# Performance work log

Hardware: AMD Instinct MI355X
Metric: run time of the kernel (lower is better)

## Reference

```python
import jax, jax.numpy as jnp
import numpy as np

B, S, HID = 2, 2048, 2048
H, KV, D = 16, 4, 128
EPS = 1e-6


def rms_norm(x, w, eps=EPS):
    # Qwen3.5 convention: (1 + weight) * RMSNorm(x), weight init 0
    v = jnp.mean(x * x, axis=-1, keepdims=True)
    return (1.0 + w) * (x * jax.lax.rsqrt(v + eps))


def rotate_half(x):
    x1, x2 = jnp.split(x, 2, axis=-1)
    return jnp.concatenate([-x2, x1], axis=-1)


def apply_rope(x, cos, sin):
    # x: [B,S,h,D]; cos/sin: [S,D]
    c = cos[None, :, None, :]
    s = sin[None, :, None, :]
    return x * c + rotate_half(x) * s


def setup_inputs():
    key = jax.random.key(0)
    ks = jax.random.split(key, 8)
    sc = 0.02
    hidden_states = jax.random.normal(ks[0], (B, S, HID), jnp.float32)
    past_key_value = jnp.zeros((B, 2, KV, S, D), jnp.float32)
    pos = jnp.arange(S, dtype=jnp.float32)
    inv_freq = 1.0 / (10000.0 ** (jnp.arange(0, D, 2, dtype=jnp.float32) / D))
    ang = pos[:, None] * inv_freq[None, :]                    # [S, D/2]
    cos = jnp.concatenate([jnp.cos(ang), jnp.cos(ang)], -1)   # [S, D]
    sin = jnp.concatenate([jnp.sin(ang), jnp.sin(ang)], -1)
    rope_rotary_cos_sin = jnp.stack([cos, sin], axis=1)       # [S, 2, D]
    context_lengths = jnp.full((B,), S, dtype=jnp.int32)
    kvcache_start_index = jnp.zeros((B,), dtype=jnp.int32)
    Wq = jax.random.normal(ks[1], (HID, H * D * 2), jnp.float32) * sc
    Wk = jax.random.normal(ks[2], (HID, KV * D), jnp.float32) * sc
    Wv = jax.random.normal(ks[3], (HID, KV * D), jnp.float32) * sc
    Wo = jax.random.normal(ks[4], (H * D, HID), jnp.float32) * sc
    q_norm_w = jax.random.normal(ks[5], (D,), jnp.float32) * sc
    k_norm_w = jax.random.normal(ks[6], (D,), jnp.float32) * sc
    return {"hidden_states": hidden_states, "past_key_value": past_key_value,
            "rope_rotary_cos_sin": rope_rotary_cos_sin,
            "context_lengths": context_lengths,
            "kvcache_start_index": kvcache_start_index,
            "Wq": Wq, "Wk": Wk, "Wv": Wv, "Wo": Wo,
            "q_norm_w": q_norm_w, "k_norm_w": k_norm_w}


def reference(hidden_states, past_key_value, rope_rotary_cos_sin,
              context_lengths, kvcache_start_index,
              Wq, Wk, Wv, Wo, q_norm_w, k_norm_w):
    # projections
    q_out = jnp.einsum('bsc,cd->bsd', hidden_states, Wq).reshape(B, S, H, 2 * D)
    query, gate = jnp.split(q_out, 2, axis=-1)                # each [B,S,H,D]
    k = jnp.einsum('bsc,cd->bsd', hidden_states, Wk).reshape(B, S, KV, D)
    v = jnp.einsum('bsc,cd->bsd', hidden_states, Wv).reshape(B, S, KV, D)
    # per-head QK RMSNorm
    query = rms_norm(query, q_norm_w)
    k = rms_norm(k, k_norm_w)
    # RoPE
    cos, sin = rope_rotary_cos_sin[:, 0, :], rope_rotary_cos_sin[:, 1, :]
    query = apply_rope(query, cos, sin)
    k = apply_rope(k, cos, sin)
    # write KV cache (prefill at start index 0)
    present = past_key_value.at[:, 0, :, :S, :].set(jnp.transpose(k, (0, 2, 1, 3)))
    present = present.at[:, 1, :, :S, :].set(jnp.transpose(v, (0, 2, 1, 3)))
    # GQA causal attention
    group = H // KV
    k_r = jnp.repeat(k, group, axis=2)                        # [B,S,H,D]
    v_r = jnp.repeat(v, group, axis=2)
    scores = jnp.einsum('bqhd,bkhd->bhqk', query, k_r) / jnp.sqrt(jnp.float32(D))
    causal = jnp.tril(jnp.ones((S, S), dtype=bool))
    scores = jnp.where(causal[None, None], scores, jnp.float32(-1e30))
    probs = jax.nn.softmax(scores, axis=-1)
    attn = jnp.einsum('bhqk,bkhd->bqhd', probs, v_r)          # [B,S,H,D]
    # sigmoid gating + output proj
    attn = attn * jax.nn.sigmoid(gate)
    out = jnp.einsum('bsd,dc->bsc', attn.reshape(B, S, H * D), Wo)
    return out, present
```

## Files before the change

### kernel.cpp

```cpp
#include <hip/hip_runtime.h>
#include <hip/hip_bf16.h>
#include <cstdint>
#include <cstddef>

#define BB   2
#define SS   2048
#define HIDD 2048
#define HH   16
#define KVH  4
#define DD   128
#define NQKV 5120
#define MM   4096

typedef unsigned short u16t;
typedef __attribute__((ext_vector_type(8))) short s16x8;
typedef __attribute__((ext_vector_type(4))) short s16x4;
typedef __attribute__((ext_vector_type(4))) float f32x4;

__device__ __forceinline__ u16t f2bf(float f) {
  unsigned u = __float_as_uint(f);
  u += 0x7fffu + ((u >> 16) & 1u);
  return (u16t)(u >> 16);
}
__device__ __forceinline__ float bf2f(u16t h) {
  return __uint_as_float(((unsigned)h) << 16);
}
__device__ __forceinline__ void gload_lds16(const void* g, void* l) {
  __builtin_amdgcn_global_load_lds(
      (const __attribute__((address_space(1))) unsigned int*)g,
      (__attribute__((address_space(3))) unsigned int*)l, 16, 0, 0);
}

__global__ __launch_bounds__(256) void cast_x(const float* __restrict__ in,
                                              u16t* __restrict__ out) {
  size_t i = ((size_t)blockIdx.x * 256 + threadIdx.x) * 4;
  f32x4 v = *(const f32x4*)(in + i);
  s16x4 o;
  o[0] = (short)f2bf(v[0]); o[1] = (short)f2bf(v[1]);
  o[2] = (short)f2bf(v[2]); o[3] = (short)f2bf(v[3]);
  *(s16x4*)(out + i) = o;
}

__global__ __launch_bounds__(256) void transpose_cast(const float* __restrict__ src,
                                                      u16t* __restrict__ dst, int N) {
  __shared__ float lds[64 * 65];
  int t = threadIdx.x;
  const int ktiles = HIDD / 64;
  int n0 = (blockIdx.x / ktiles) << 6;
  int k0 = (blockIdx.x % ktiles) << 6;
#pragma unroll
  for (int i = 0; i < 16; i++) {
    int idx = i * 256 + t;
    int r = idx >> 6, c = idx & 63;
    lds[c * 65 + r] = src[(size_t)(k0 + r) * N + n0 + c];
  }
  __syncthreads();
#pragma unroll
  for (int i = 0; i < 16; i++) {
    int idx = i * 256 + t;
    int rr = idx >> 6, kk = idx & 63;
    dst[(size_t)(n0 + rr) * HIDD + k0 + kk] = f2bf(lds[rr * 65 + kk]);
  }
}

__device__ __forceinline__ s16x8 ldsfrag(const char* half, int r, int g) {
  return *(const s16x8*)(half + r * 64 + ((g ^ ((r >> 1) & 3)) << 4));
}
__device__ __forceinline__ void stage_half(char* ldsbase, const u16t* gbase,
                                           int K, int kcol, int tid) {
#pragma unroll
  for (int i = 0; i < 2; i++) {
    int o16 = i * 512 + tid;
    int r = o16 >> 2;
    int cs = (o16 & 3) ^ ((r >> 1) & 3);
    gload_lds16(gbase + (size_t)r * K + kcol + cs * 8, ldsbase + o16 * 16);
  }
}

template <typename CT>
__global__ __launch_bounds__(512, 2) void gemm8(const u16t* __restrict__ A,
                                                const u16t* __restrict__ Bt,
                                                CT* __restrict__ C,
                                                int M, int N, int K) {
  extern __shared__ __align__(16) char lds[];
  char* As = lds;
  char* Bs = lds + 65536;
  int tid = threadIdx.x, lane = tid & 63, w = tid >> 6;
  int wm = w >> 2, wn = w & 3;
  int cpx = gridDim.x >> 3;
  int wgid = (blockIdx.x & 7) * cpx + (blockIdx.x >> 3);
  int bm = wgid & 15, bn = wgid >> 4;
  int m0 = bm << 8, n0 = bn << 8;
  const u16t* Ag = A + (size_t)m0 * K;
  const u16t* Bg = Bt + (size_t)n0 * K;
  const int NT = K >> 6;

  stage_half(As, Ag, K, 0, tid);
  stage_half(Bs, Bg, K, 0, tid);
  stage_half(As + 16384, Ag, K, 32, tid);
  stage_half(Bs + 16384, Bg, K, 32, tid);
  stage_half(As + 32768, Ag, K, 64, tid);
  stage_half(Bs + 32768, Bg, K, 64, tid);
  asm volatile("s_waitcnt vmcnt(8)" ::: "memory");
  __builtin_amdgcn_s_barrier();

  const f32x4 fz = {0.f, 0.f, 0.f, 0.f};
  f32x4 acc[8][4];
#pragma unroll
  for (int i = 0; i < 8; i++)
#pragma unroll
    for (int j = 0; j < 4; j++) acc[i][j] = fz;
  s16x8 afr[4], bfr[4];
  int g = lane >> 4;
  int rA = (lane & 15) + wm * 128;
  int rB = (lane & 15) + wn * 64;

  for (int kt = 0; kt < NT; kt++) {
    int cur = kt & 1;
    char* Acur = As + cur * 32768;
    char* Bcur = Bs + cur * 32768;
    char* Anxt = As + (cur ^ 1) * 32768;
    char* Bnxt = Bs + (cur ^ 1) * 32768;
#pragma unroll
    for (int ni = 0; ni < 4; ni++) bfr[ni] = ldsfrag(Bcur, rB + ni * 16, g);
#pragma unroll
    for (int mi = 0; mi < 4; mi++) afr[mi] = ldsfrag(Acur, rA + mi * 16, g);
    if (kt + 1 < NT) stage_half(Anxt + 16384, Ag, K, (kt + 1) * 64 + 32, tid);
    __builtin_amdgcn_s_barrier();
    asm volatile("s_waitcnt lgkmcnt(0)" ::: "memory");
    __builtin_amdgcn_s_setprio(1);
#pragma unroll
    for (int mi = 0; mi < 4; mi++)
#pragma unroll
      for (int ni = 0; ni < 4; ni++)
        acc[mi][ni] = __builtin_amdgcn_mfma_f32_16x16x32_bf16(afr[mi], bfr[ni], acc[mi][ni], 0, 0, 0);
    __builtin_amdgcn_s_setprio(0);
    __builtin_amdgcn_s_barrier();
#pragma unroll
    for (int mi = 0; mi < 4; mi++) afr[mi] = ldsfrag(Acur, rA + 64 + mi * 16, g);
    if (kt + 1 < NT) stage_half(Bnxt + 16384, Bg, K, (kt + 1) * 64 + 32, tid);
    __builtin_amdgcn_s_barrier();
    asm volatile("s_waitcnt lgkmcnt(0)" ::: "memory");
    __builtin_amdgcn_s_setprio(1);
#pragma unroll
    for (int mi = 0; mi < 4; mi++)
#pragma unroll
      for (int ni = 0; ni < 4; ni++)
        acc[4 + mi][ni] = __builtin_amdgcn_mfma_f32_16x16x32_bf16(afr[mi], bfr[ni], acc[4 + mi][ni], 0, 0, 0);
    __builtin_amdgcn_s_setprio(0);
    if (kt + 1 < NT) asm volatile("s_waitcnt vmcnt(8)" ::: "memory");
    else             asm volatile("s_waitcnt vmcnt(0)" ::: "memory");
    __builtin_amdgcn_s_barrier();
#pragma unroll
    for (int ni = 0; ni < 4; ni++) bfr[ni] = ldsfrag(Bcur + 16384, rB + ni * 16, g);
#pragma unroll
    for (int mi = 0; mi < 4; mi++) afr[mi] = ldsfrag(Acur + 16384, rA + mi * 16, g);
    if (kt + 2 < NT) stage_half(Acur, Ag, K, (kt + 2) * 64, tid);
    __builtin_amdgcn_s_barrier();
    asm volatile("s_waitcnt lgkmcnt(0)" ::: "memory");
    __builtin_amdgcn_s_setprio(1);
#pragma unroll
    for (int mi = 0; mi < 4; mi++)
#pragma unroll
      for (int ni = 0; ni < 4; ni++)
        acc[mi][ni] = __builtin_amdgcn_mfma_f32_16x16x32_bf16(afr[mi], bfr[ni], acc[mi][ni], 0, 0, 0);
    __builtin_amdgcn_s_setprio(0);
    __builtin_amdgcn_s_barrier();
#pragma unroll
    for (int mi = 0; mi < 4; mi++) afr[mi] = ldsfrag(Acur + 16384, rA + 64 + mi * 16, g);
    if (kt + 2 < NT) stage_half(Bcur, Bg, K, (kt + 2) * 64, tid);
    __builtin_amdgcn_s_barrier();
    asm volatile("s_waitcnt lgkmcnt(0)" ::: "memory");
    __builtin_amdgcn_s_setprio(1);
#pragma unroll
    for (int mi = 0; mi < 4; mi++)
#pragma unroll
      for (int ni = 0; ni < 4; ni++)
        acc[4 + mi][ni] = __builtin_amdgcn_mfma_f32_16x16x32_bf16(afr[mi], bfr[ni], acc[4 + mi][ni], 0, 0, 0);
    __builtin_amdgcn_s_setprio(0);
    if (kt < NT - 1) {
      if (kt + 2 < NT) asm volatile("s_waitcnt vmcnt(8)" ::: "memory");
      else             asm volatile("s_waitcnt vmcnt(4)" ::: "memory");
    }
    __builtin_amdgcn_s_barrier();
  }
#pragma unroll
  for (int mi = 0; mi < 8; mi++)
#pragma unroll
    for (int ni = 0; ni < 4; ni++) {
      int row0 = m0 + wm * 128 + mi * 16 + ((lane >> 4) << 2);
      int col = n0 + wn * 64 + ni * 16 + (lane & 15);
#pragma unroll
      for (int j = 0; j < 4; j++) {
        if constexpr (sizeof(CT) == 2)
          C[(size_t)(row0 + j) * N + col] = f2bf(acc[mi][ni][j]);
        else
          C[(size_t)(row0 + j) * N + col] = acc[mi][ni][j];
      }
    }
}

template <typename CT>
__global__ __launch_bounds__(256) void gemm_bt(const u16t* __restrict__ A,
                                               const u16t* __restrict__ Bt,
                                               CT* __restrict__ C,
                                               int M, int N, int K) {
  __shared__ __align__(16) char As[128 * 64];
  __shared__ __align__(16) char Bs[128 * 64];
  int tid = threadIdx.x;
  int lane = tid & 63;
  int w = tid >> 6;
  int cpx = gridDim.x >> 3;
  int wgid = ((int)blockIdx.x & 7) * cpx + ((int)blockIdx.x >> 3);
  int mtiles = M >> 7;
  int bm = wgid % mtiles;
  int bn = wgid / mtiles;
  int m0 = bm << 7, n0 = bn << 7;
  int wr = (w >> 1) * 64, wc = (w & 1) * 64;

  const f32x4 fz = {0.f, 0.f, 0.f, 0.f};
  f32x4 acc[4][4];
#pragma unroll
  for (int i = 0; i < 4; i++)
#pragma unroll
    for (int j = 0; j < 4; j++) acc[i][j] = fz;

  for (int k0 = 0; k0 < K; k0 += 32) {
    __syncthreads();
#pragma unroll
    for (int i = 0; i < 2; i++) {
      int idx = i * 256 + tid;
      int r = idx >> 2, c = idx & 3;
      int csrc = c ^ ((r >> 1) & 3);
      gload_lds16(A + (size_t)(m0 + r) * K + k0 + csrc * 8, As + idx * 16);
      gload_lds16(Bt + (size_t)(n0 + r) * K + k0 + csrc * 8, Bs + idx * 16);
    }
    __syncthreads();
    s16x8 af[4], bf[4];
    int g = lane >> 4;
#pragma unroll
    for (int mi = 0; mi < 4; mi++) {
      int r = wr + mi * 16 + (lane & 15);
      af[mi] = *(const s16x8*)(As + r * 64 + ((g ^ ((r >> 1) & 3)) << 4));
    }
#pragma unroll
    for (int ni = 0; ni < 4; ni++) {
      int r = wc + ni * 16 + (lane & 15);
      bf[ni] = *(const s16x8*)(Bs + r * 64 + ((g ^ ((r >> 1) & 3)) << 4));
    }
#pragma unroll
    for (int mi = 0; mi < 4; mi++)
#pragma unroll
      for (int ni = 0; ni < 4; ni++)
        acc[mi][ni] = __builtin_amdgcn_mfma_f32_16x16x32_bf16(af[mi], bf[ni], acc[mi][ni], 0, 0, 0);
  }
#pragma unroll
  for (int mi = 0; mi < 4; mi++)
#pragma unroll
    for (int ni = 0; ni < 4; ni++) {
      int row0 = m0 + wr + mi * 16 + ((lane >> 4) << 2);
      int col = n0 + wc + ni * 16 + (lane & 15);
#pragma unroll
      for (int j = 0; j < 4; j++) {
        if constexpr (sizeof(CT) == 2)
          C[(size_t)(row0 + j) * N + col] = f2bf(acc[mi][ni][j]);
        else
          C[(size_t)(row0 + j) * N + col] = acc[mi][ni][j];
      }
    }
}

__global__ __launch_bounds__(256) void qk_norm_rope(const u16t* __restrict__ Cqkv,
                                                    const float* __restrict__ rope,
                                                    const float* __restrict__ qw,
                                                    const float* __restrict__ kw,
                                                    u16t* __restrict__ Qb,
                                                    u16t* __restrict__ Kb,
                                                    u16t* __restrict__ Gs,
                                                    float* __restrict__ present) {
  int wid = blockIdx.x * 4 + (threadIdx.x >> 6);
  int lane = threadIdx.x & 63;
  const int NQ = BB * SS * HH;
  if (wid < NQ) {
    int b = wid >> 15;
    int rem = wid & 32767;
    int s = rem >> 4, h = rem & 15;
    const u16t* base = Cqkv + (size_t)(b * SS + s) * NQKV + h * 256;
    float xlo = bf2f(base[lane]), xhi = bf2f(base[64 + lane]);
    float ss = xlo * xlo + xhi * xhi;
    ss += __shfl_xor(ss, 1);  ss += __shfl_xor(ss, 2);  ss += __shfl_xor(ss, 4);
    ss += __shfl_xor(ss, 8);  ss += __shfl_xor(ss, 16); ss += __shfl_xor(ss, 32);
    float r = rsqrtf(ss * (1.f / 128.f) + 1e-6f);
    float qlo = xlo * r * (1.f + qw[lane]);
    float qhi = xhi * r * (1.f + qw[64 + lane]);
    const float* cs = rope + (size_t)s * 256;
    float clo = cs[lane], chi = cs[64 + lane];
    float slo = cs[128 + lane], shi = cs[192 + lane];
    const float SC = 0.08838834764831845f;
    float olo = (qlo * clo - qhi * slo) * SC;
    float ohi = (qhi * chi + qlo * shi) * SC;
    size_t qoff = (((size_t)b * HH + h) * SS + s) * DD;
    Qb[qoff + lane] = f2bf(olo);
    Qb[qoff + 64 + lane] = f2bf(ohi);
    float glo = bf2f(base[128 + lane]), ghi = bf2f(base[192 + lane]);
    size_t goff = ((size_t)(b * SS + s)) * (HH * DD) + h * DD;
    Gs[goff + lane] = f2bf(1.f / (1.f + __expf(-glo)));
    Gs[goff + 64 + lane] = f2bf(1.f / (1.f + __expf(-ghi)));
  } else {
    int wid2 = wid - NQ;
    int b = wid2 >> 13;
    int rem = wid2 & 8191;
    int s = rem >> 2, kv = rem & 3;
    const u16t* base = Cqkv + (size_t)(b * SS + s) * NQKV + 4096 + kv * 128;
    float xlo = bf2f(base[lane]), xhi = bf2f(base[64 + lane]);
    float ss = xlo * xlo + xhi * xhi;
    ss += __shfl_xor(ss, 1);  ss += __shfl_xor(ss, 2);  ss += __shfl_xor(ss, 4);
    ss += __shfl_xor(ss, 8);  ss += __shfl_xor(ss, 16); ss += __shfl_xor(ss, 32);
    float r = rsqrtf(ss * (1.f / 128.f) + 1e-6f);
    float klo = xlo * r * (1.f + kw[lane]);
    float khi = xhi * r * (1.f + kw[64 + lane]);
    const float* cs = rope + (size_t)s * 256;
    float clo = cs[lane], chi = cs[64 + lane];
    float slo = cs[128 + lane], shi = cs[192 + lane];
    float olo = klo * clo - khi * slo;
    float ohi = khi * chi + klo * shi;
    size_t koff = (((size_t)b * KVH + kv) * SS + s) * DD;
    Kb[koff + lane] = f2bf(olo);
    Kb[koff + 64 + lane] = f2bf(ohi);
    size_t poff = (((size_t)(b * 2 * KVH + kv)) * SS + s) * DD;
    present[poff + lane] = olo;
    present[poff + 64 + lane] = ohi;
  }
}

__global__ __launch_bounds__(256) void v_write(const u16t* __restrict__ Cqkv,
                                               float* __restrict__ present,
                                               u16t* __restrict__ Vtb) {
  __shared__ float lds[128 * 65];
  int t = threadIdx.x;
  int b = blockIdx.x >> 7;
  int kv = (blockIdx.x >> 5) & 3;
  int s0 = (blockIdx.x & 31) << 6;
#pragma unroll
  for (int i = 0; i < 32; i++) {
    int idx = i * 256 + t;
    int sp = idx >> 7, d = idx & 127;
    float v = bf2f(Cqkv[(size_t)(b * SS + s0 + sp) * NQKV + 4608 + kv * 128 + d]);
    present[(((size_t)(b * 2 * KVH + KVH + kv)) * SS + s0 + sp) * DD + d] = v;
    lds[d * 65 + sp] = v;
  }
  __syncthreads();
#pragma unroll
  for (int i = 0; i < 8; i++) {
    int d = i * 16 + (t >> 4);
    int sp = (t & 15) * 4;
    s16x4 pk;
    pk[0] = (short)f2bf(lds[d * 65 + sp + 0]);
    pk[1] = (short)f2bf(lds[d * 65 + sp + 1]);
    pk[2] = (short)f2bf(lds[d * 65 + sp + 2]);
    pk[3] = (short)f2bf(lds[d * 65 + sp + 3]);
    *(s16x4*)(Vtb + ((size_t)(b * KVH + kv) * DD + d) * SS + s0 + sp) = pk;
  }
}

__global__ __launch_bounds__(256) void attn_kernel(const u16t* __restrict__ Qb,
                                                   const u16t* __restrict__ Kb,
                                                   const u16t* __restrict__ Vtb,
                                                   const u16t* __restrict__ Gs,
                                                   u16t* __restrict__ AttG) {
  __shared__ __align__(16) char Ks[2][16384];
  __shared__ __align__(16) char Vs[2][16384];
  __shared__ __align__(16) char Ps[4 * 2048];

  int tid = threadIdx.x, lane = tid & 63, w = tid >> 6;
  int x = blockIdx.x & 7;
  int b = x >> 2, kv = x & 3;
  int rr = blockIdx.x >> 3;
  int h = kv * 4 + (rr & 3);
  int p = rr >> 2;

  const u16t* Kbase = Kb + (((size_t)(b * KVH + kv)) * SS) * DD;
  const u16t* Vbase = Vtb + (((size_t)(b * KVH + kv)) * DD) * SS;

  auto stageK = [&](int kt, int buf) {
#pragma unroll
    for (int i = 0; i < 4; i++) {
      int idx = i * 256 + tid;
      int r_ = idx >> 4, c_ = idx & 15;
      gload_lds16(Kbase + (size_t)(kt * 64 + r_) * DD + (c_ ^ (r_ & 7)) * 8, Ks[buf] + idx * 16);
    }
  };
  auto stageV = [&](int kt, int buf) {
#pragma unroll
    for (int i = 0; i < 4; i++) {
      int idx = i * 256 + tid;
      int r_ = idx >> 3, c_ = idx & 7;
      gload_lds16(Vbase + (size_t)r_ * SS + kt * 64 + (c_ ^ (r_ & 7)) * 8, Vs[buf] + idx * 16);
    }
  };

  const f32x4 fz = {0.f, 0.f, 0.f, 0.f};
  char* pbase = Ps + w * 2048;
  int cur = 0;

  stageK(0, 0);
  stageV(0, 0);

  for (int seg = 0; seg < 2; seg++) {
    int qt = (seg == 0) ? (31 - p) : p;
    const u16t* Qbase = Qb + (((size_t)(b * HH + h)) * SS + qt * 64) * DD;
    s16x8 qf[4];
    {
      const u16t* qrow = Qbase + (size_t)(w * 16 + (lane & 15)) * DD + (lane >> 4) * 8;
#pragma unroll
      for (int ks = 0; ks < 4; ks++) qf[ks] = *(const s16x8*)(qrow + ks * 32);
    }
    f32x4 acco[8];
#pragma unroll
    for (int f = 0; f < 8; f++) acco[f] = fz;
    float mrun[4], lrun[4];
#pragma unroll
    for (int j = 0; j < 4; j++) { mrun[j] = -INFINITY; lrun[j] = 0.f; }

    if (seg == 0) {
      asm volatile("s_waitcnt vmcnt(0)" ::: "memory");
      __builtin_amdgcn_s_barrier();
    }

    for (int kt = 0; kt <= qt; kt++) {
      bool havenext = (kt < qt) || (seg == 0);
      if (havenext) {
        int nk = (kt < qt) ? (kt + 1) : 0;
        stageK(nk, cur ^ 1);
        stageV(nk, cur ^ 1);
      }
      f32x4 accs[4];
#pragma unroll
      for (int ni = 0; ni < 4; ni++) accs[ni] = fz;
#pragma unroll
      for (int ni = 0; ni < 4; ni++) {
        int r = ni * 16 + (lane & 15);
#pragma unroll
        for (int ks = 0; ks < 4; ks++) {
          int g = ks * 4 + (lane >> 4);
          s16x8 bfk = *(const s16x8*)(Ks[cur] + r * 256 + ((g ^ (r & 7)) << 4));
          accs[ni] = __builtin_amdgcn_mfma_f32_16x16x32_bf16(qf[ks], bfk, accs[ni], 0, 0, 0);
        }
      }
      if (kt == qt) {
#pragma unroll
        for (int ni = 0; ni < 4; ni++) {
          int col = ni * 16 + (lane & 15);
#pragma unroll
          for (int j = 0; j < 4; j++) {
            int row = w * 16 + ((lane >> 4) << 2) + j;
            if (col > row) accs[ni][j] = -1e30f;
          }
        }
      }
      float mt[4];
#pragma unroll
      for (int j = 0; j < 4; j++) {
        float v = fmaxf(fmaxf(accs[0][j], accs[1][j]), fmaxf(accs[2][j], accs[3][j]));
        v = fmaxf(v, __shfl_xor(v, 1));
        v = fmaxf(v, __shfl_xor(v, 2));
        v = fmaxf(v, __shfl_xor(v, 4));
        v = fmaxf(v, __shfl_xor(v, 8));
        mt[j] = v;
      }
      float alpha[4];
#pragma unroll
      for (int j = 0; j < 4; j++) {
        float mnew = fmaxf(mrun[j], mt[j]);
        alpha[j] = __expf(mrun[j] - mnew);
        mrun[j] = mnew;
      }
      float rs[4] = {0.f, 0.f, 0.f, 0.f};
#pragma unroll
      for (int ni = 0; ni < 4; ni++)
#pragma unroll
        for (int j = 0; j < 4; j++) {
          float pv = __expf(accs[ni][j] - mrun[j]);
          accs[ni][j] = pv;
          rs[j] += pv;
        }
#pragma unroll
      for (int j = 0; j < 4; j++) {
        float v = rs[j];
        v += __shfl_xor(v, 1); v += __shfl_xor(v, 2);
        v += __shfl_xor(v, 4); v += __shfl_xor(v, 8);
        lrun[j] = lrun[j] * alpha[j] + v;
      }
#pragma unroll
      for (int f = 0; f < 8; f++)
#pragma unroll
        for (int j = 0; j < 4; j++) acco[f][j] *= alpha[j];

#pragma unroll
      for (int ni = 0; ni < 4; ni++)
#pragma unroll
        for (int j = 0; j < 4; j++) {
          int row = ((lane >> 4) << 2) + j, col = ni * 16 + (lane & 15);
          int ch = (col >> 3) ^ (row & 7);
          *(u16t*)(pbase + row * 128 + ch * 16 + (col & 7) * 2) = f2bf(accs[ni][j]);
        }
#pragma unroll
      for (int ks = 0; ks < 2; ks++) {
        int pr = lane & 15;
        int pch = (ks * 4 + (lane >> 4)) ^ (pr & 7);
        s16x8 pa = *(const s16x8*)(pbase + pr * 128 + (pch << 4));
#pragma unroll
        for (int f = 0; f < 8; f++) {
          int d = f * 16 + (lane & 15);
          int g = ks * 4 + (lane >> 4);
          s16x8 vf = *(const s16x8*)(Vs[cur] + d * 128 + ((g ^ (d & 7)) << 4));
          acco[f] = __builtin_amdgcn_mfma_f32_16x16x32_bf16(pa, vf, acco[f], 0, 0, 0);
        }
      }
      if (havenext) {
        asm volatile("s_waitcnt vmcnt(0)" ::: "memory");
        __builtin_amdgcn_s_barrier();
        cur ^= 1;
      }
    }
#pragma unroll
    for (int f = 0; f < 8; f++) {
      int d = f * 16 + (lane & 15);
#pragma unroll
      for (int j = 0; j < 4; j++) {
        int srow = qt * 64 + w * 16 + ((lane >> 4) << 2) + j;
        float o = acco[f][j] / lrun[j];
        size_t off = ((size_t)b * SS + srow) * (HH * DD) + h * DD + d;
        float g = bf2f(Gs[off]);
        AttG[off] = f2bf(o * g);
      }
    }
  }
}

extern "C" void kernel_launch(void* const* d_in, const int* in_sizes, int n_in,
                              void* d_out, int out_size, void* d_ws, size_t ws_size,
                              hipStream_t stream) {
  const float* hidden = (const float*)d_in[0];
  const float* rope   = (const float*)d_in[2];
  const float* Wq     = (const float*)d_in[5];
  const float* Wk     = (const float*)d_in[6];
  const float* Wv     = (const float*)d_in[7];
  const float* Wo     = (const float*)d_in[8];
  const float* qw     = (const float*)d_in[9];
  const float* kw     = (const float*)d_in[10];
  float* out = (float*)d_out;
  float* present = out + (size_t)BB * SS * HIDD;

  char* ws = (char*)d_ws;
  u16t* Xb    = (u16t*)(ws);
  u16t* Wt    = (u16t*)(ws + 16777216);
  u16t* Wot   = (u16t*)(ws + 37748736);
  u16t* Cqkv  = (u16t*)(ws + 46137344);
  u16t* Qb    = (u16t*)(ws + 88080384);
  u16t* Kb    = (u16t*)(ws + 104857600);
  u16t* Vtb   = (u16t*)(ws + 109051904);
  u16t* Gs    = (u16t*)(ws + 113246208);
  u16t* AttG  = Xb;

  (void)hipFuncSetAttribute(reinterpret_cast<const void*>(gemm8<u16t>),
                            hipFuncAttributeMaxDynamicSharedMemorySize, 131072);

  cast_x<<<8192, 256, 0, stream>>>(hidden, Xb);
  transpose_cast<<<(4096 / 64) * 32, 256, 0, stream>>>(Wq, Wt, 4096);
  transpose_cast<<<(512 / 64) * 32, 256, 0, stream>>>(Wk, Wt + (size_t)4096 * HIDD, 512);
  transpose_cast<<<(512 / 64) * 32, 256, 0, stream>>>(Wv, Wt + (size_t)4608 * HIDD, 512);
  transpose_cast<<<(2048 / 64) * 32, 256, 0, stream>>>(Wo, Wot, 2048);
  gemm8<u16t><<<(MM / 256) * (4096 / 256), 512, 131072, stream>>>(Xb, Wt, Cqkv, MM, NQKV, HIDD);
  gemm_bt<u16t><<<(MM / 128) * (1024 / 128), 256, 0, stream>>>(
      Xb, Wt + (size_t)4096 * HIDD, Cqkv + 4096, MM, NQKV, HIDD);
  qk_norm_rope<<<(BB * SS * (HH + KVH)) / 4, 256, 0, stream>>>(Cqkv, rope, qw, kw, Qb, Kb, Gs, present);
  v_write<<<BB * KVH * (SS / 64), 256, 0, stream>>>(Cqkv, present, Vtb);
  attn_kernel<<<BB * HH * (SS / 128), 256, 0, stream>>>(Qb, Kb, Vtb, Gs, AttG);
  gemm_bt<float><<<(MM / 128) * (HIDD / 128), 256, 0, stream>>>(AttG, Wot, out, MM, HIDD, HIDD);
}
```

Baseline: 309.9 us.

## Transpose QK^T MFMA so each lane owns one query row, use exp2 softmax

```diff
diff --git a/kernel.cpp b/kernel.cpp
--- a/kernel.cpp
+++ b/kernel.cpp
@@ -29,6 +29,17 @@
   __builtin_amdgcn_global_load_lds(
       (const __attribute__((address_space(1))) unsigned int*)g,
       (__attribute__((address_space(3))) unsigned int*)l, 16, 0, 0);
+}
+__device__ __forceinline__ unsigned cvtpk_bf16(float lo, float hi) {
+  unsigned r;
+  asm("v_cvt_pk_bf16_f32 %0, %1, %2" : "=v"(r) : "v"(lo), "v"(hi));
+  return r;
+}
+__device__ __forceinline__ f32x4 fmax4(f32x4 a, f32x4 b) {
+  f32x4 r;
+  r[0] = fmaxf(a[0], b[0]); r[1] = fmaxf(a[1], b[1]);
+  r[2] = fmaxf(a[2], b[2]); r[3] = fmaxf(a[3], b[3]);
+  return r;
 }
 
 __global__ __launch_bounds__(256) void cast_x(const float* __restrict__ in,
@@ -296,7 +307,7 @@
     const float* cs = rope + (size_t)s * 256;
     float clo = cs[lane], chi = cs[64 + lane];
     float slo = cs[128 + lane], shi = cs[192 + lane];
-    const float SC = 0.08838834764831845f;
+    const float SC = 0.08838834764831845f * 1.4426950408889634f;
     float olo = (qlo * clo - qhi * slo) * SC;
     float ohi = (qhi * chi + qlo * shi) * SC;
     size_t qoff = (((size_t)b * HH + h) * SS + s) * DD;
@@ -400,7 +411,10 @@
   };
 
   const f32x4 fz = {0.f, 0.f, 0.f, 0.f};
-  char* pbase = Ps + w * 2048;
+  int g = lane >> 4;
+  int q15 = lane & 15;
+  int q7 = q15 & 7;
+  char* pq = Ps + w * 2048 + q15 * 128;
   int cur = 0;
 
   stageK(0, 0);
@@ -411,16 +425,14 @@
     const u16t* Qbase = Qb + (((size_t)(b * HH + h)) * SS + qt * 64) * DD;
     s16x8 qf[4];
     {
-      const u16t* qrow = Qbase + (size_t)(w * 16 + (lane & 15)) * DD + (lane >> 4) * 8;
+      const u16t* qrow = Qbase + (size_t)(w * 16 + q15) * DD + g * 8;
 #pragma unroll
       for (int ks = 0; ks < 4; ks++) qf[ks] = *(const s16x8*)(qrow + ks * 32);
     }
     f32x4 acco[8];
 #pragma unroll
     for (int f = 0; f < 8; f++) acco[f] = fz;
-    float mrun[4], lrun[4];
-#pragma unroll
-    for (int j = 0; j < 4; j++) { mrun[j] = -INFINITY; lrun[j] = 0.f; }
+    float mrun = -INFINITY, lrun = 0.f;
 
     if (seg == 0) {
       asm volatile("s_waitcnt vmcnt(0)" ::: "memory");
@@ -439,81 +451,67 @@
       for (int ni = 0; ni < 4; ni++) accs[ni] = fz;
 #pragma unroll
       for (int ni = 0; ni < 4; ni++) {
-        int r = ni * 16 + (lane & 15);
+        int r = ni * 16 + q15;
 #pragma unroll
         for (int ks = 0; ks < 4; ks++) {
-          int g = ks * 4 + (lane >> 4);
-          s16x8 bfk = *(const s16x8*)(Ks[cur] + r * 256 + ((g ^ (r & 7)) << 4));
-          accs[ni] = __builtin_amdgcn_mfma_f32_16x16x32_bf16(qf[ks], bfk, accs[ni], 0, 0, 0);
+          int g2 = ks * 4 + g;
+          s16x8 bfk = *(const s16x8*)(Ks[cur] + r * 256 + ((g2 ^ (r & 7)) << 4));
+          accs[ni] = __builtin_amdgcn_mfma_f32_16x16x32_bf16(bfk, qf[ks], accs[ni], 0, 0, 0);
         }
       }
       if (kt == qt) {
-#pragma unroll
-        for (int ni = 0; ni < 4; ni++) {
-          int col = ni * 16 + (lane & 15);
+        int ql = w * 16 + q15;
+#pragma unroll
+        for (int ni = 0; ni < 4; ni++)
 #pragma unroll
           for (int j = 0; j < 4; j++) {
-            int row = w * 16 + ((lane >> 4) << 2) + j;
-            if (col > row) accs[ni][j] = -1e30f;
+            int kl = ni * 16 + (g << 2) + j;
+            if (kl > ql) accs[ni][j] = -1e30f;
           }
+      }
+      f32x4 m4 = fmax4(fmax4(accs[0], accs[1]), fmax4(accs[2], accs[3]));
+      float mt = fmaxf(fmaxf(m4[0], m4[1]), fmaxf(m4[2], m4[3]));
+      mt = fmaxf(mt, __shfl_xor(mt, 16));
+      mt = fmaxf(mt, __shfl_xor(mt, 32));
+      float mnew = fmaxf(mrun, mt);
+      float alpha = __builtin_amdgcn_exp2f(mrun - mnew);
+      mrun = mnew;
+      float rs = 0.f;
+#pragma unroll
+      for (int ni = 0; ni < 4; ni++)
+#pragma unroll
+        for (int j = 0; j < 4; j++) {
+          float pv = __builtin_amdgcn_exp2f(accs[ni][j] - mnew);
+          accs[ni][j] = pv;
+          rs += pv;
         }
-      }
-      float mt[4];
-#pragma unroll
-      for (int j = 0; j < 4; j++) {
-        float v = fmaxf(fmaxf(accs[0][j], accs[1][j]), fmaxf(accs[2][j], accs[3][j]));
-        v = fmaxf(v, __shfl_xor(v, 1));
-        v = fmaxf(v, __shfl_xor(v, 2));
-        v = fmaxf(v, __shfl_xor(v, 4));
-        v = fmaxf(v, __shfl_xor(v, 8));
-        mt[j] = v;
-      }
-      float alpha[4];
-#pragma unroll
-      for (int j = 0; j < 4; j++) {
-        float mnew = fmaxf(mrun[j], mt[j]);
-        alpha[j] = __expf(mrun[j] - mnew);
-        mrun[j] = mnew;
-      }
-      float rs[4] = {0.f, 0.f, 0.f, 0.f};
-#pragma unroll
-      for (int ni = 0; ni < 4; ni++)
-#pragma unroll
-        for (int j = 0; j < 4; j++) {
-          float pv = __expf(accs[ni][j] - mrun[j]);
-          accs[ni][j] = pv;
-          rs[j] += pv;
+      rs += __shfl_xor(rs, 16);
+      rs += __shfl_xor(rs, 32);
+      lrun = lrun * alpha + rs;
+      float ar[4];
+#pragma unroll
+      for (int j = 0; j < 4; j++) ar[j] = __shfl(alpha, (g << 2) + j);
+#pragma unroll
+      for (int f = 0; f < 8; f++)
+#pragma unroll
+        for (int j = 0; j < 4; j++) acco[f][j] *= ar[j];
+
+#pragma unroll
+      for (int ni = 0; ni < 4; ni++)
+#pragma unroll
+        for (int jj = 0; jj < 2; jj++) {
+          unsigned pk32 = cvtpk_bf16(accs[ni][2 * jj], accs[ni][2 * jj + 1]);
+          int gr = ni * 2 + (g >> 1);
+          int off = ((gr ^ q7) << 4) + ((g & 1) << 3) + (jj << 2);
+          *(unsigned*)(pq + off) = pk32;
         }
 #pragma unroll
-      for (int j = 0; j < 4; j++) {
-        float v = rs[j];
-        v += __shfl_xor(v, 1); v += __shfl_xor(v, 2);
-        v += __shfl_xor(v, 4); v += __shfl_xor(v, 8);
-        lrun[j] = lrun[j] * alpha[j] + v;
-      }
-#pragma unroll
-      for (int f = 0; f < 8; f++)
-#pragma unroll
-        for (int j = 0; j < 4; j++) acco[f][j] *= alpha[j];
-
-#pragma unroll
-      for (int ni = 0; ni < 4; ni++)
-#pragma unroll
-        for (int j = 0; j < 4; j++) {
-          int row = ((lane >> 4) << 2) + j, col = ni * 16 + (lane & 15);
-          int ch = (col >> 3) ^ (row & 7);
-          *(u16t*)(pbase + row * 128 + ch * 16 + (col & 7) * 2) = f2bf(accs[ni][j]);
-        }
-#pragma unroll
-      for (int ks = 0; ks < 2; ks++) {
-        int pr = lane & 15;
-        int pch = (ks * 4 + (lane >> 4)) ^ (pr & 7);
-        s16x8 pa = *(const s16x8*)(pbase + pr * 128 + (pch << 4));
+      for (int ks2 = 0; ks2 < 2; ks2++) {
+        s16x8 pa = *(const s16x8*)(pq + (((ks2 * 4 + g) ^ q7) << 4));
 #pragma unroll
         for (int f = 0; f < 8; f++) {
-          int d = f * 16 + (lane & 15);
-          int g = ks * 4 + (lane >> 4);
-          s16x8 vf = *(const s16x8*)(Vs[cur] + d * 128 + ((g ^ (d & 7)) << 4));
+          int d = f * 16 + q15;
+          s16x8 vf = *(const s16x8*)(Vs[cur] + d * 128 + (((ks2 * 4 + g) ^ (d & 7)) << 4));
           acco[f] = __builtin_amdgcn_mfma_f32_16x16x32_bf16(pa, vf, acco[f], 0, 0, 0);
         }
       }
@@ -523,16 +521,19 @@
         cur ^= 1;
       }
     }
+    float lr[4];
+#pragma unroll
+    for (int j = 0; j < 4; j++) lr[j] = __shfl(lrun, (g << 2) + j);
 #pragma unroll
     for (int f = 0; f < 8; f++) {
-      int d = f * 16 + (lane & 15);
+      int d = f * 16 + q15;
 #pragma unroll
       for (int j = 0; j < 4; j++) {
-        int srow = qt * 64 + w * 16 + ((lane >> 4) << 2) + j;
-        float o = acco[f][j] / lrun[j];
+        int srow = qt * 64 + w * 16 + (g << 2) + j;
+        float o = acco[f][j] / lr[j];
         size_t off = ((size_t)b * SS + srow) * (HH * DD) + h * DD + d;
-        float g = bf2f(Gs[off]);
-        AttG[off] = f2bf(o * g);
+        float gt = bf2f(Gs[off]);
+        AttG[off] = f2bf(o * gt);
       }
     }
   }
```

After: 291.9 us. 1.06x faster.
